# Optimization experiments

Hardware: AMD Instinct MI355X
Metric: run time of the kernel (lower is better)

The kernel has to match this reference:

```python
import jax, jax.numpy as jnp
import numpy as np

NUM_NODES = 50000
NUM_EDGES = 800000
NUM_FEATURES = 128
HIDDEN = 256
NUM_CLASSES = 10
NUM_GRAPHS = 64


def setup_inputs() -> dict:
    key = jax.random.key(0)
    ks = jax.random.split(key, 16)
    x = jax.random.normal(ks[0], (NUM_NODES, NUM_FEATURES), dtype=jnp.float32)
    edge_index = jax.random.randint(ks[1], (2, NUM_EDGES), 0, NUM_NODES, dtype=jnp.int64)
    batch = jnp.sort(jax.random.randint(ks[2], (NUM_NODES,), 0, NUM_GRAPHS, dtype=jnp.int64))

    def glorot(k, shape):
        fan_in, fan_out = shape[-2], shape[-1]
        s = jnp.sqrt(6.0 / (fan_in + fan_out)).astype(jnp.float32)
        return jax.random.uniform(k, shape, jnp.float32, -s, s)

    inp = {
        "x": x, "edge_index": edge_index, "batch": batch,
        # Chebyshev weights: one [in, out] matrix per hop order k
        "W1": glorot(ks[3], (3, NUM_FEATURES, HIDDEN)), "b1": jnp.zeros((HIDDEN,), jnp.float32),
        "W2": glorot(ks[4], (4, HIDDEN, HIDDEN)),       "b2": jnp.zeros((HIDDEN,), jnp.float32),
        "W3": glorot(ks[5], (5, HIDDEN, HIDDEN)),       "b3": jnp.zeros((HIDDEN,), jnp.float32),
        "fc1_w": glorot(ks[6], (HIDDEN, 512)),  "fc1_b": jnp.zeros((512,), jnp.float32),
        "fc2_w": glorot(ks[7], (512, HIDDEN)),  "fc2_b": jnp.zeros((HIDDEN,), jnp.float32),
        "fc3_w": glorot(ks[8], (HIDDEN, NUM_CLASSES)), "fc3_b": jnp.zeros((NUM_CLASSES,), jnp.float32),
    }
    return inp


def reference(x, edge_index, batch, W1, b1, W2, b2, W3, b3,
              fc1_w, fc1_b, fc2_w, fc2_b, fc3_w, fc3_b):
    N = x.shape[0]
    src, dst = edge_index[0], edge_index[1]

    # Scaled Laplacian L_hat = -D^{-1/2} A D^{-1/2} (lambda_max = 2, sym norm)
    deg = jax.ops.segment_sum(jnp.ones_like(src, dtype=x.dtype), src, num_segments=N)
    dis = jnp.where(deg > 0, jax.lax.rsqrt(jnp.maximum(deg, 1.0)), 0.0)
    w = -dis[src] * dis[dst]  # [E]

    def prop(h):  # L_hat @ h via gather-scale-scatter
        return jax.ops.segment_sum(h[src] * w[:, None], dst, num_segments=N)

    def cheb(h, Wk, b):
        K = Wk.shape[0]
        Tx0 = h
        out = Tx0 @ Wk[0]
        Tx1 = prop(h)
        out = out + Tx1 @ Wk[1]
        for k in range(2, K):
            Tx2 = 2.0 * prop(Tx1) - Tx0
            out = out + Tx2 @ Wk[k]
            Tx0, Tx1 = Tx1, Tx2
        return out + b

    h = jax.nn.relu(cheb(x, W1, b1))
    h = jax.nn.relu(cheb(h, W2, b2))
    h = jax.nn.relu(cheb(h, W3, b3))

    # global mean pool over graphs in the batch
    sums = jax.ops.segment_sum(h, batch, num_segments=NUM_GRAPHS)
    cnts = jax.ops.segment_sum(jnp.ones((N,), h.dtype), batch, num_segments=NUM_GRAPHS)
    g = sums / jnp.maximum(cnts, 1.0)[:, None]  # [G, 256]

    g = jax.nn.relu(g @ fc1_w + fc1_b)  # dropout is identity at inference
    g = jax.nn.relu(g @ fc2_w + fc2_b)
    g = g @ fc3_w + fc3_b
    return jax.nn.log_softmax(g, axis=1)
```

## Files before the change

### kernel.cpp

```cpp
#include <hip/hip_runtime.h>
#include <cstdint>
#include <cstddef>

#define NN 50000
#define NE 800000
#define FIN 128
#define HID 256
#define NCLS 10
#define NG 64
#define LDT 1280

#define NCH 13
#define NCELL (NN * NCH)
#define NSCB ((NCELL + 255) / 256)

typedef unsigned int uint;
typedef unsigned short ushort;
typedef __attribute__((ext_vector_type(8))) short short8;
typedef __attribute__((ext_vector_type(4))) float f32x4;

static inline size_t align_up(size_t v, size_t a) { return (v + a - 1) / a * a; }

__device__ __forceinline__ float bf2f(ushort u) {
    union { uint i; float f; } v; v.i = (uint)u << 16; return v.f;
}
__device__ __forceinline__ ushort f2bf(float f) {
    union { uint i; float f; } v; v.f = f;
    uint i = v.i;
    uint r = (i + 0x7fffu + ((i >> 16) & 1u)) >> 16;
    return (ushort)r;
}
__device__ __forceinline__ uint pack2(float a, float b) {
    return (uint)f2bf(a) | ((uint)f2bf(b) << 16);
}


__global__ void k_degcnt(const int* __restrict__ src, const int* __restrict__ dst,
                         int* __restrict__ ideg, int* __restrict__ cellcnt) {
    int e = blockIdx.x * 256 + threadIdx.x;
    if (e < NE) {
        int s = src[e], d = dst[e];
        atomicAdd(&ideg[s], 1);
        atomicAdd(&cellcnt[d * NCH + (s >> 12)], 1);
    }
}

__global__ void k_dis(const int* __restrict__ ideg, float* __restrict__ dis) {
    int n = blockIdx.x * 256 + threadIdx.x;
    if (n < NN) {
        int d = ideg[n];
        dis[n] = (d > 0) ? rsqrtf((float)d) : 0.0f;
    }
}

__global__ void k_scanA(const int* __restrict__ cnt, int* __restrict__ rp,
                        int* __restrict__ bsum) {
    __shared__ int s[256];
    int i = blockIdx.x * 256 + threadIdx.x;
    int v = (i < NCELL) ? cnt[i] : 0;
    s[threadIdx.x] = v;
    __syncthreads();
    for (int off = 1; off < 256; off <<= 1) {
        int t = (threadIdx.x >= (unsigned)off) ? s[threadIdx.x - off] : 0;
        __syncthreads();
        s[threadIdx.x] += t;
        __syncthreads();
    }
    if (i < NCELL) rp[i] = s[threadIdx.x] - v;
    if (threadIdx.x == 255) bsum[blockIdx.x] = s[255];
}

__global__ void k_scanB(int* __restrict__ b, int n) {
    __shared__ int s[1024];
    __shared__ int carry;
    if (threadIdx.x == 0) carry = 0;
    __syncthreads();
    for (int base = 0; base < n; base += 1024) {
        int i = base + threadIdx.x;
        int v = (i < n) ? b[i] : 0;
        s[threadIdx.x] = v;
        __syncthreads();
        for (int off = 1; off < 1024; off <<= 1) {
            int t = (threadIdx.x >= (unsigned)off) ? s[threadIdx.x - off] : 0;
            __syncthreads();
            s[threadIdx.x] += t;
            __syncthreads();
        }
        int c = carry;
        if (i < n) b[i] = c + s[threadIdx.x] - v;
        __syncthreads();
        if (threadIdx.x == 0) carry = c + s[1023];
        __syncthreads();
    }
}

__global__ void k_scanC(const int* __restrict__ bsum, int* __restrict__ rp,
                        int* __restrict__ cur, int* __restrict__ rpn) {
    int i = blockIdx.x * 256 + threadIdx.x;
    if (i < NCELL) {
        int v = rp[i] + bsum[blockIdx.x];
        rp[i] = v;
        cur[i] = v;
        if (i % NCH == 0) rpn[i / NCH] = v;
    }
    if (i == 0) rpn[NN] = NE;
}

__global__ void k_fill2(const int* __restrict__ src, const int* __restrict__ dst,
                        const float* __restrict__ dis, int* __restrict__ cur,
                        uint2* __restrict__ em) {
    int e = blockIdx.x * 256 + threadIdx.x;
    if (e < NE) {
        int s = src[e], d = dst[e];
        int pos = atomicAdd(&cur[d * NCH + (s >> 12)], 1);
        uint2 m;
        m.x = (uint)s;
        m.y = __float_as_uint(-dis[s] * dis[d]);
        em[pos] = m;
    }
}

__global__ void k_wtall(const float* __restrict__ W1, const float* __restrict__ W2,
                        const float* __restrict__ W3, ushort* __restrict__ Wt1,
                        ushort* __restrict__ Wt2, ushort* __restrict__ Wt3) {
    int i = blockIdx.x * 256 + threadIdx.x;
    if (i < 384 * 256) {
        int k = i >> 8, n = i & 255;
        Wt1[(size_t)n * 384 + k] = f2bf(W1[i]);
        return;
    }
    i -= 384 * 256;
    if (i < 1024 * 256) {
        int k = i >> 8, n = i & 255;
        Wt2[(size_t)n * 1024 + k] = f2bf(W2[i]);
        return;
    }
    i -= 1024 * 256;
    if (i < 1280 * 256) {
        int k = i >> 8, n = i & 255;
        Wt3[(size_t)n * 1280 + k] = f2bf(W3[i]);
    }
}


__global__ void k_spread_x(const float* __restrict__ x, ushort* __restrict__ T) {
    int i = blockIdx.x * 256 + threadIdx.x;
    if (i < NN * 64) {
        int m = i >> 6, p = i & 63;
        const float* xp = x + (size_t)m * FIN + p * 2;
        uint* tp = (uint*)(T + (size_t)m * LDT) + p;
        *tp = pack2(xp[0], xp[1]);
    }
}

template <int FUSE, int F>
__global__ __launch_bounds__(512) void k_prop3(
    const int* __restrict__ rpn, const uint2* __restrict__ em,
    const ushort* __restrict__ h, const ushort* __restrict__ sub,
    ushort* __restrict__ out) {
    constexpr int NV = (F == 256) ? 4 : 2;
    int wv = __builtin_amdgcn_readfirstlane(threadIdx.x >> 6);
    int d = blockIdx.x * 8 + wv;
    int lane = threadIdx.x & 63;
    int beg = rpn[d], end = rpn[d + 1];
    float a[NV];
#pragma unroll
    for (int j = 0; j < NV; ++j) a[j] = 0.0f;

    int e = beg;
    int nfull = (end - beg) >> 3;
    if (nfull > 0) {
        uint2 mt[8];
#pragma unroll
        for (int u = 0; u < 8; ++u) mt[u] = em[e + u];
        for (int g = 0; g < nfull; ++g) {
            uint2 mtn[8];
            if (F == 256) {
                uint2 gg[8];
#pragma unroll
                for (int u = 0; u < 8; ++u)
                    gg[u] = *((const uint2*)(h + (size_t)mt[u].x * LDT) + lane);
#pragma unroll
                for (int u = 0; u < 8; ++u) {
                    int pe = e + 8 + u; if (pe > end - 1) pe = end - 1;
                    mtn[u] = em[pe];
                }
#pragma unroll
                for (int u = 0; u < 8; ++u) {
                    float wvv = __uint_as_float(mt[u].y);
                    a[0] += wvv * bf2f((ushort)gg[u].x);
                    a[1] += wvv * bf2f((ushort)(gg[u].x >> 16));
                    a[2] += wvv * bf2f((ushort)gg[u].y);
                    a[3] += wvv * bf2f((ushort)(gg[u].y >> 16));
                }
            } else {
                uint gg[8];
#pragma unroll
                for (int u = 0; u < 8; ++u)
                    gg[u] = *((const uint*)(h + (size_t)mt[u].x * LDT) + lane);
#pragma unroll
                for (int u = 0; u < 8; ++u) {
                    int pe = e + 8 + u; if (pe > end - 1) pe = end - 1;
                    mtn[u] = em[pe];
                }
#pragma unroll
                for (int u = 0; u < 8; ++u) {
                    float wvv = __uint_as_float(mt[u].y);
                    a[0] += wvv * bf2f((ushort)gg[u]);
                    a[1] += wvv * bf2f((ushort)(gg[u] >> 16));
                }
            }
#pragma unroll
            for (int u = 0; u < 8; ++u) mt[u] = mtn[u];
            e += 8;
        }
    }
    for (; e + 4 <= end; e += 4) {
        uint2 mt[4];
#pragma unroll
        for (int u = 0; u < 4; ++u) mt[u] = em[e + u];
        if (F == 256) {
            uint2 gg[4];
#pragma unroll
            for (int u = 0; u < 4; ++u)
                gg[u] = *((const uint2*)(h + (size_t)mt[u].x * LDT) + lane);
#pragma unroll
            for (int u = 0; u < 4; ++u) {
                float wvv = __uint_as_float(mt[u].y);
                a[0] += wvv * bf2f((ushort)gg[u].x);
                a[1] += wvv * bf2f((ushort)(gg[u].x >> 16));
                a[2] += wvv * bf2f((ushort)gg[u].y);
                a[3] += wvv * bf2f((ushort)(gg[u].y >> 16));
            }
        } else {
            uint gg[4];
#pragma unroll
            for (int u = 0; u < 4; ++u)
                gg[u] = *((const uint*)(h + (size_t)mt[u].x * LDT) + lane);
#pragma unroll
            for (int u = 0; u < 4; ++u) {
                float wvv = __uint_as_float(mt[u].y);
                a[0] += wvv * bf2f((ushort)gg[u]);
                a[1] += wvv * bf2f((ushort)(gg[u] >> 16));
            }
        }
    }
    for (; e < end; ++e) {
        uint2 m0 = em[e];
        float w0 = __uint_as_float(m0.y);
        if (F == 256) {
            uint2 g0 = *((const uint2*)(h + (size_t)m0.x * LDT) + lane);
            a[0] += w0 * bf2f((ushort)g0.x); a[1] += w0 * bf2f((ushort)(g0.x >> 16));
            a[2] += w0 * bf2f((ushort)g0.y); a[3] += w0 * bf2f((ushort)(g0.y >> 16));
        } else {
            uint g0 = *((const uint*)(h + (size_t)m0.x * LDT) + lane);
            a[0] += w0 * bf2f((ushort)g0); a[1] += w0 * bf2f((ushort)(g0 >> 16));
        }
    }

    if (F == 256) {
        uint2* op = (uint2*)(out + (size_t)d * LDT) + lane;
        if (FUSE) {
            uint2 sv = *((const uint2*)(sub + (size_t)d * LDT) + lane);
            uint2 r;
            r.x = pack2(2.0f * a[0] - bf2f((ushort)sv.x),
                        2.0f * a[1] - bf2f((ushort)(sv.x >> 16)));
            r.y = pack2(2.0f * a[2] - bf2f((ushort)sv.y),
                        2.0f * a[3] - bf2f((ushort)(sv.y >> 16)));
            *op = r;
        } else {
            uint2 r;
            r.x = pack2(a[0], a[1]);
            r.y = pack2(a[2], a[3]);
            *op = r;
        }
    } else {
        uint* op = (uint*)(out + (size_t)d * LDT) + lane;
        if (FUSE) {
            uint sv = *((const uint*)(sub + (size_t)d * LDT) + lane);
            *op = pack2(2.0f * a[0] - bf2f((ushort)sv),
                        2.0f * a[1] - bf2f((ushort)(sv >> 16)));
        } else {
            *op = pack2(a[0], a[1]);
        }
    }
}

template <int K>
__global__ __launch_bounds__(512, 4) void k_mm7(
    const ushort* __restrict__ A, int lda,
    int m0, int m1, int m2, int m3, int m4,
    const ushort* __restrict__ Wt, const float* __restrict__ bias,
    ushort* __restrict__ H, int ldh, int M) {
    constexpr int NT = K / 32;
    __shared__ ushort As[3][128 * 32];
    __shared__ ushort Bs[3][256 * 32];
    int tid = threadIdx.x;
    int lane = tid & 63, w = tid >> 6;
    int wm = w >> 2, wn = w & 3;
    int rowBase = blockIdx.x * 128;
    int srow = lane >> 2;
    int c16 = lane & 3;

    f32x4 acc[4][4];
#pragma unroll
    for (int i = 0; i < 4; ++i)
#pragma unroll
        for (int j = 0; j < 4; ++j) acc[i][j] = (f32x4){0.f, 0.f, 0.f, 0.f};

    auto stage = [&](int t) {
        int kk = t * 32;
        int slot = kk >> 8;
        int coff = (slot == 0 ? m0 : slot == 1 ? m1 : slot == 2 ? m2
                    : slot == 3 ? m3 : m4) + (kk & 255);
        int b = t % 3;
        {
            int r = w * 16 + srow;
            int cs = c16 ^ ((r >> 1) & 3);
            int grow = rowBase + r;
            if (grow > M - 1) grow = M - 1;
            const ushort* gp = A + (size_t)grow * lda + coff + cs * 8;
            __builtin_amdgcn_global_load_lds(
                (const __attribute__((address_space(1))) void*)gp,
                (__attribute__((address_space(3))) void*)((char*)&As[b][0] + w * 1024),
                16, 0, 0);
        }
#pragma unroll
        for (int q = 0; q < 2; ++q) {
            int seg = w * 2 + q;
            int r = seg * 16 + srow;
            int cs = c16 ^ ((r >> 1) & 3);
            const ushort* gp = Wt + (size_t)r * K + kk + cs * 8;
            __builtin_amdgcn_global_load_lds(
                (const __attribute__((address_space(1))) void*)gp,
                (__attribute__((address_space(3))) void*)((char*)&Bs[b][0] + seg * 1024),
                16, 0, 0);
        }
    };

    stage(0);
    stage(1);

    for (int t = 0; t < NT; ++t) {
        if (t + 1 < NT) {
            asm volatile("s_waitcnt vmcnt(3)" ::: "memory");
        } else {
            asm volatile("s_waitcnt vmcnt(0)" ::: "memory");
        }
        __builtin_amdgcn_s_barrier();
        if (t + 2 < NT) stage(t + 2);

        int b = t % 3;
        short8 af[4], bf[4];
#pragma unroll
        for (int mi = 0; mi < 4; ++mi) {
            int r = wm * 64 + mi * 16 + (lane & 15);
            int j = (lane >> 4) ^ ((r >> 1) & 3);
            af[mi] = *(const short8*)((const char*)&As[b][0] + r * 64 + j * 16);
        }
#pragma unroll
        for (int ni = 0; ni < 4; ++ni) {
            int r = wn * 64 + ni * 16 + (lane & 15);
            int j = (lane >> 4) ^ ((r >> 1) & 3);
            bf[ni] = *(const short8*)((const char*)&Bs[b][0] + r * 64 + j * 16);
        }
#pragma unroll
        for (int mi = 0; mi < 4; ++mi)
#pragma unroll
            for (int ni = 0; ni < 4; ++ni)
                acc[mi][ni] = __builtin_amdgcn_mfma_f32_16x16x32_bf16(
                    af[mi], bf[ni], acc[mi][ni], 0, 0, 0);
    }

    int lg = lane >> 4;
    float bv[4];
#pragma unroll
    for (int ni = 0; ni < 4; ++ni)
        bv[ni] = bias[wn * 64 + ni * 16 + (lane & 15)];
#pragma unroll
    for (int mi = 0; mi < 4; ++mi) {
#pragma unroll
        for (int r = 0; r < 4; ++r) {
            int row = rowBase + wm * 64 + mi * 16 + lg * 4 + r;
            if (row >= M) continue;
#pragma unroll
            for (int ni = 0; ni < 4; ++ni) {
                int colL = wn * 64 + ni * 16 + (lane & 15);
                float v = acc[mi][ni][r] + bv[ni];
                v = fmaxf(v, 0.0f);
                H[(size_t)row * ldh + colL] = f2bf(v);
            }
        }
    }
}


__global__ void k_pool(const ushort* __restrict__ h, const int* __restrict__ batch,
                       float* __restrict__ sums, float* __restrict__ cnts) {
    int f = threadIdx.x;
    int n0 = blockIdx.x * 128;
    if (n0 >= NN) return;
    int nEnd = n0 + 128 < NN ? n0 + 128 : NN;
    int cur = batch[n0];
    float acc = 0.0f, c = 0.0f;
    for (int n = n0; n < nEnd; ++n) {
        int b = batch[n];
        if (b != cur) {
            atomicAdd(&sums[cur * HID + f], acc);
            if (f == 0) atomicAdd(&cnts[cur], c);
            acc = 0.0f; c = 0.0f; cur = b;
        }
        acc += bf2f(h[(size_t)n * HID + f]);
        c += 1.0f;
    }
    atomicAdd(&sums[cur * HID + f], acc);
    if (f == 0) atomicAdd(&cnts[cur], c);
}

__global__ void k_gdiv(const float* __restrict__ sums, const float* __restrict__ cnts,
                       float* __restrict__ g) {
    int i = blockIdx.x * 256 + threadIdx.x;
    int b = i >> 8;
    g[i] = sums[i] / fmaxf(cnts[b], 1.0f);
}


template <int RELU>
__global__ void k_fc(const float* __restrict__ in, const float* __restrict__ W,
                     const float* __restrict__ bias, float* __restrict__ out,
                     int K, int Nc) {
    __shared__ float s[512];
    int gi = blockIdx.x;
    for (int i = threadIdx.x; i < K; i += blockDim.x) s[i] = in[gi * K + i];
    __syncthreads();
    int c = blockIdx.y * blockDim.x + threadIdx.x;
    if (c < Nc) {
        float acc = bias[c];
        for (int k = 0; k < K; ++k) acc += s[k] * W[k * Nc + c];
        out[gi * Nc + c] = RELU ? fmaxf(acc, 0.0f) : acc;
    }
}

__global__ void k_fc3_lsm(const float* __restrict__ in, const float* __restrict__ W,
                          const float* __restrict__ b, float* __restrict__ out) {
    __shared__ float s[HID];
    __shared__ float lg[NCLS];
    int gi = blockIdx.x;
    s[threadIdx.x] = in[gi * HID + threadIdx.x];
    __syncthreads();
    if (threadIdx.x < NCLS) {
        float acc = b[threadIdx.x];
        for (int k = 0; k < HID; ++k) acc += s[k] * W[k * NCLS + threadIdx.x];
        lg[threadIdx.x] = acc;
    }
    __syncthreads();
    if (threadIdx.x < NCLS) {
        float m = -1e30f;
        for (int c = 0; c < NCLS; ++c) m = fmaxf(m, lg[c]);
        float sum = 0.0f;
        for (int c = 0; c < NCLS; ++c) sum += expf(lg[c] - m);
        out[gi * NCLS + threadIdx.x] = lg[threadIdx.x] - m - logf(sum);
    }
}


extern "C" void kernel_launch(void* const* d_in, const int* in_sizes, int n_in,
                              void* d_out, int out_size, void* d_ws, size_t ws_size,
                              hipStream_t stream) {
    const float* x = (const float*)d_in[0];
    const int* ei = (const int*)d_in[1];
    const int* src = ei;
    const int* dst = ei + NE;
    const int* batch = (const int*)d_in[2];
    const float* W1 = (const float*)d_in[3];
    const float* b1 = (const float*)d_in[4];
    const float* W2 = (const float*)d_in[5];
    const float* b2 = (const float*)d_in[6];
    const float* W3 = (const float*)d_in[7];
    const float* b3 = (const float*)d_in[8];
    const float* fc1w = (const float*)d_in[9];
    const float* fc1b = (const float*)d_in[10];
    const float* fc2w = (const float*)d_in[11];
    const float* fc2b = (const float*)d_in[12];
    const float* fc3w = (const float*)d_in[13];
    const float* fc3b = (const float*)d_in[14];
    float* out = (float*)d_out;

    char* p = (char*)d_ws;
    auto carve = [&](size_t bytes) {
        char* r = p;
        p += align_up(bytes, 256);
        return (void*)r;
    };
    ushort* Tbig = (ushort*)carve((size_t)NN * LDT * 2);
    ushort* hA = (ushort*)carve((size_t)NN * HID * 2);
    ushort* Wt1 = (ushort*)carve((size_t)HID * 384 * 2);
    ushort* Wt2 = (ushort*)carve((size_t)HID * 1024 * 2);
    ushort* Wt3 = (ushort*)carve((size_t)HID * 1280 * 2);
    int* ideg = (int*)carve((size_t)NN * 4);
    float* dis = (float*)carve((size_t)NN * 4);
    uint2* em = (uint2*)carve((size_t)NE * 8);
    int* cellcnt = (int*)carve((size_t)NCELL * 4);
    int* cellptr = (int*)carve((size_t)(NCELL + 1) * 4);
    int* ccur = (int*)carve((size_t)NCELL * 4);
    int* rpn = (int*)carve((size_t)(NN + 1) * 4);
    int* bsum = (int*)carve((size_t)NSCB * 4);
    float* psum = (float*)carve((size_t)NG * HID * 4);
    float* pcnt = (float*)carve((size_t)NG * 4);
    float* g = (float*)carve((size_t)NG * HID * 4);
    float* f1 = (float*)carve((size_t)NG * 512 * 4);
    float* f2 = (float*)carve((size_t)NG * HID * 4);

    hipMemsetAsync(ideg, 0, (size_t)NN * 4, stream);
    hipMemsetAsync(cellcnt, 0, (size_t)NCELL * 4, stream);
    hipMemsetAsync(psum, 0, (size_t)NG * HID * 4, stream);
    hipMemsetAsync(pcnt, 0, (size_t)NG * 4, stream);

    k_degcnt<<<(NE + 255) / 256, 256, 0, stream>>>(src, dst, ideg, cellcnt);
    k_dis<<<(NN + 255) / 256, 256, 0, stream>>>(ideg, dis);
    k_scanA<<<NSCB, 256, 0, stream>>>(cellcnt, cellptr, bsum);
    k_scanB<<<1, 1024, 0, stream>>>(bsum, NSCB);
    k_scanC<<<NSCB, 256, 0, stream>>>(bsum, cellptr, ccur, rpn);
    k_fill2<<<(NE + 255) / 256, 256, 0, stream>>>(src, dst, dis, ccur, em);

    k_wtall<<<(384 + 1024 + 1280), 256, 0, stream>>>(W1, W2, W3, Wt1, Wt2, Wt3);

    int mmg = (NN + 127) / 128;

    k_spread_x<<<(NN * 64 + 255) / 256, 256, 0, stream>>>(x, Tbig);
    k_prop3<0, 128><<<NN / 8, 512, 0, stream>>>(rpn, em, Tbig + 0, nullptr, Tbig + 128);
    k_prop3<1, 128><<<NN / 8, 512, 0, stream>>>(rpn, em, Tbig + 128, Tbig + 0, Tbig + 256);
    k_mm7<384><<<mmg, 512, 0, stream>>>(Tbig, LDT, 0, 256, 0, 0, 0,
                                        Wt1, b1, Tbig + 1024, LDT, NN);

    k_prop3<0, 256><<<NN / 8, 512, 0, stream>>>(rpn, em, Tbig + 1024, nullptr, Tbig + 0);
    k_prop3<1, 256><<<NN / 8, 512, 0, stream>>>(rpn, em, Tbig + 0, Tbig + 1024, Tbig + 256);
    k_prop3<1, 256><<<NN / 8, 512, 0, stream>>>(rpn, em, Tbig + 256, Tbig + 0, Tbig + 512);
    k_mm7<1024><<<mmg, 512, 0, stream>>>(Tbig, LDT, 1024, 0, 256, 512, 0,
                                         Wt2, b2, Tbig + 768, LDT, NN);

    k_prop3<0, 256><<<NN / 8, 512, 0, stream>>>(rpn, em, Tbig + 768, nullptr, Tbig + 1024);
    k_prop3<1, 256><<<NN / 8, 512, 0, stream>>>(rpn, em, Tbig + 1024, Tbig + 768, Tbig + 0);
    k_prop3<1, 256><<<NN / 8, 512, 0, stream>>>(rpn, em, Tbig + 0, Tbig + 1024, Tbig + 256);
    k_prop3<1, 256><<<NN / 8, 512, 0, stream>>>(rpn, em, Tbig + 256, Tbig + 0, Tbig + 512);
    k_mm7<1280><<<mmg, 512, 0, stream>>>(Tbig, LDT, 768, 1024, 0, 256, 512,
                                         Wt3, b3, hA, HID, NN);

    k_pool<<<(NN + 127) / 128, 256, 0, stream>>>(hA, batch, psum, pcnt);
    k_gdiv<<<(NG * HID) / 256, 256, 0, stream>>>(psum, pcnt, g);
    k_fc<1><<<dim3(NG, 2), 256, 0, stream>>>(g, fc1w, fc1b, f1, HID, 512);
    k_fc<1><<<dim3(NG, 1), 256, 0, stream>>>(f1, fc2w, fc2b, f2, 512, HID);
    k_fc3_lsm<<<NG, 256, 0, stream>>>(f2, fc3w, fc3b, out);
}
```

Measured before the change: 799.7 us.

## Shrink edge metadata to source indices and split 256-wide propagation across two waves

Edges now store only the source index. The per-edge weight is rebuilt in the propagation kernels from dis[src] and a per-destination -dis[d] factor applied once after accumulation. Cell counters and cursors are packed as 16-bit halves of 32-bit words, halving their footprint and removing the cursor copy in the scan. The 256-feature propagation gives each destination two wavefronts, each handling 128 features with 32-bit gathers and a deeper 16-edge unroll, which doubles the grid. The changes trade per-edge metadata bandwidth for an extra dependent gather of dis per edge, and the 16-bit counters assume no cell exceeds 65535 edges.

After: 1.136 ms. +42.1%, slower.

```diff
diff --git a/kernel.cpp b/kernel.cpp
--- a/kernel.cpp
+++ b/kernel.cpp
@@ -36,12 +36,13 @@
 
 
 __global__ void k_degcnt(const int* __restrict__ src, const int* __restrict__ dst,
-                         int* __restrict__ ideg, int* __restrict__ cellcnt) {
+                         int* __restrict__ ideg, uint* __restrict__ cellcnt32) {
     int e = blockIdx.x * 256 + threadIdx.x;
     if (e < NE) {
         int s = src[e], d = dst[e];
         atomicAdd(&ideg[s], 1);
-        atomicAdd(&cellcnt[d * NCH + (s >> 12)], 1);
+        int cell = d * NCH + (s >> 12);
+        atomicAdd(&cellcnt32[cell >> 1], 1u << ((cell & 1) * 16));
     }
 }
 
@@ -53,11 +54,12 @@
     }
 }
 
-__global__ void k_scanA(const int* __restrict__ cnt, int* __restrict__ rp,
+__global__ void k_scanA(const uint* __restrict__ cnt32, int* __restrict__ rp,
                         int* __restrict__ bsum) {
     __shared__ int s[256];
     int i = blockIdx.x * 256 + threadIdx.x;
-    int v = (i < NCELL) ? cnt[i] : 0;
+    int v = 0;
+    if (i < NCELL) v = (int)((cnt32[i >> 1] >> ((i & 1) * 16)) & 0xffffu);
     s[threadIdx.x] = v;
     __syncthreads();
     for (int off = 1; off < 256; off <<= 1) {
@@ -95,28 +97,26 @@
 }
 
 __global__ void k_scanC(const int* __restrict__ bsum, int* __restrict__ rp,
-                        int* __restrict__ cur, int* __restrict__ rpn) {
+                        int* __restrict__ rpn) {
     int i = blockIdx.x * 256 + threadIdx.x;
     if (i < NCELL) {
         int v = rp[i] + bsum[blockIdx.x];
         rp[i] = v;
-        cur[i] = v;
         if (i % NCH == 0) rpn[i / NCH] = v;
     }
     if (i == 0) rpn[NN] = NE;
 }
 
 __global__ void k_fill2(const int* __restrict__ src, const int* __restrict__ dst,
-                        const float* __restrict__ dis, int* __restrict__ cur,
-                        uint2* __restrict__ em) {
+                        const int* __restrict__ cellptr, uint* __restrict__ cur32,
+                        uint* __restrict__ em) {
     int e = blockIdx.x * 256 + threadIdx.x;
     if (e < NE) {
         int s = src[e], d = dst[e];
-        int pos = atomicAdd(&cur[d * NCH + (s >> 12)], 1);
-        uint2 m;
-        m.x = (uint)s;
-        m.y = __float_as_uint(-dis[s] * dis[d]);
-        em[pos] = m;
+        int cell = d * NCH + (s >> 12);
+        uint old = atomicAdd(&cur32[cell >> 1], 1u << ((cell & 1) * 16));
+        int loc = (int)((old >> ((cell & 1) * 16)) & 0xffffu);
+        em[cellptr[cell] + loc] = (uint)s;
     }
 }
 
@@ -153,136 +153,117 @@
     }
 }
 
-template <int FUSE, int F>
-__global__ __launch_bounds__(512) void k_prop3(
-    const int* __restrict__ rpn, const uint2* __restrict__ em,
-    const ushort* __restrict__ h, const ushort* __restrict__ sub,
-    ushort* __restrict__ out) {
-    constexpr int NV = (F == 256) ? 4 : 2;
-    int wv = __builtin_amdgcn_readfirstlane(threadIdx.x >> 6);
-    int d = blockIdx.x * 8 + wv;
+template <int FUSE>
+__global__ __launch_bounds__(512) void k_prop256(
+    const int* __restrict__ rpn, const uint* __restrict__ em,
+    const float* __restrict__ dis, const ushort* __restrict__ h,
+    const ushort* __restrict__ sub, ushort* __restrict__ out) {
+    int tid = threadIdx.x;
+    int d = blockIdx.x * 4 + (tid >> 7);
+    int half = (tid >> 6) & 1;
+    int lane = tid & 63;
+    int cidx = half * 64 + lane;
+    int beg = rpn[d], end = rpn[d + 1];
+    float disd = -dis[d];
+    float a0 = 0.0f, a1 = 0.0f;
+
+    int e = beg;
+    int nfull = (end - beg) >> 4;
+    for (int g = 0; g < nfull; ++g) {
+        int sv[16]; float ds[16]; uint gg[16];
+#pragma unroll
+        for (int u = 0; u < 16; ++u) sv[u] = (int)em[e + u];
+#pragma unroll
+        for (int u = 0; u < 16; ++u) ds[u] = dis[sv[u]];
+#pragma unroll
+        for (int u = 0; u < 16; ++u)
+            gg[u] = *((const uint*)(h + (size_t)sv[u] * LDT) + cidx);
+#pragma unroll
+        for (int u = 0; u < 16; ++u) {
+            a0 += ds[u] * bf2f((ushort)gg[u]);
+            a1 += ds[u] * bf2f((ushort)(gg[u] >> 16));
+        }
+        e += 16;
+    }
+    for (; e + 4 <= end; e += 4) {
+        int sv[4]; float ds[4]; uint gg[4];
+#pragma unroll
+        for (int u = 0; u < 4; ++u) sv[u] = (int)em[e + u];
+#pragma unroll
+        for (int u = 0; u < 4; ++u) ds[u] = dis[sv[u]];
+#pragma unroll
+        for (int u = 0; u < 4; ++u)
+            gg[u] = *((const uint*)(h + (size_t)sv[u] * LDT) + cidx);
+#pragma unroll
+        for (int u = 0; u < 4; ++u) {
+            a0 += ds[u] * bf2f((ushort)gg[u]);
+            a1 += ds[u] * bf2f((ushort)(gg[u] >> 16));
+        }
+    }
+    for (; e < end; ++e) {
+        int s = (int)em[e];
+        float dsv = dis[s];
+        uint g0 = *((const uint*)(h + (size_t)s * LDT) + cidx);
+        a0 += dsv * bf2f((ushort)g0);
+        a1 += dsv * bf2f((ushort)(g0 >> 16));
+    }
+
+    a0 *= disd; a1 *= disd;
+    uint* op = (uint*)(out + (size_t)d * LDT) + cidx;
+    if (FUSE) {
+        uint sv = *((const uint*)(sub + (size_t)d * LDT) + cidx);
+        *op = pack2(2.0f * a0 - bf2f((ushort)sv),
+                    2.0f * a1 - bf2f((ushort)(sv >> 16)));
+    } else {
+        *op = pack2(a0, a1);
+    }
+}
+
+template <int FUSE>
+__global__ __launch_bounds__(512) void k_prop128(
+    const int* __restrict__ rpn, const uint* __restrict__ em,
+    const float* __restrict__ dis, const ushort* __restrict__ h,
+    const ushort* __restrict__ sub, ushort* __restrict__ out) {
+    int d = blockIdx.x * 8 + (threadIdx.x >> 6);
     int lane = threadIdx.x & 63;
     int beg = rpn[d], end = rpn[d + 1];
-    float a[NV];
-#pragma unroll
-    for (int j = 0; j < NV; ++j) a[j] = 0.0f;
+    float disd = -dis[d];
+    float a0 = 0.0f, a1 = 0.0f;
 
     int e = beg;
     int nfull = (end - beg) >> 3;
-    if (nfull > 0) {
-        uint2 mt[8];
-#pragma unroll
-        for (int u = 0; u < 8; ++u) mt[u] = em[e + u];
-        for (int g = 0; g < nfull; ++g) {
-            uint2 mtn[8];
-            if (F == 256) {
-                uint2 gg[8];
-#pragma unroll
-                for (int u = 0; u < 8; ++u)
-                    gg[u] = *((const uint2*)(h + (size_t)mt[u].x * LDT) + lane);
-#pragma unroll
-                for (int u = 0; u < 8; ++u) {
-                    int pe = e + 8 + u; if (pe > end - 1) pe = end - 1;
-                    mtn[u] = em[pe];
-                }
-#pragma unroll
-                for (int u = 0; u < 8; ++u) {
-                    float wvv = __uint_as_float(mt[u].y);
-                    a[0] += wvv * bf2f((ushort)gg[u].x);
-                    a[1] += wvv * bf2f((ushort)(gg[u].x >> 16));
-                    a[2] += wvv * bf2f((ushort)gg[u].y);
-                    a[3] += wvv * bf2f((ushort)(gg[u].y >> 16));
-                }
-            } else {
-                uint gg[8];
-#pragma unroll
-                for (int u = 0; u < 8; ++u)
-                    gg[u] = *((const uint*)(h + (size_t)mt[u].x * LDT) + lane);
-#pragma unroll
-                for (int u = 0; u < 8; ++u) {
-                    int pe = e + 8 + u; if (pe > end - 1) pe = end - 1;
-                    mtn[u] = em[pe];
-                }
-#pragma unroll
-                for (int u = 0; u < 8; ++u) {
-                    float wvv = __uint_as_float(mt[u].y);
-                    a[0] += wvv * bf2f((ushort)gg[u]);
-                    a[1] += wvv * bf2f((ushort)(gg[u] >> 16));
-                }
-            }
-#pragma unroll
-            for (int u = 0; u < 8; ++u) mt[u] = mtn[u];
-            e += 8;
-        }
-    }
-    for (; e + 4 <= end; e += 4) {
-        uint2 mt[4];
-#pragma unroll
-        for (int u = 0; u < 4; ++u) mt[u] = em[e + u];
-        if (F == 256) {
-            uint2 gg[4];
-#pragma unroll
-            for (int u = 0; u < 4; ++u)
-                gg[u] = *((const uint2*)(h + (size_t)mt[u].x * LDT) + lane);
-#pragma unroll
-            for (int u = 0; u < 4; ++u) {
-                float wvv = __uint_as_float(mt[u].y);
-                a[0] += wvv * bf2f((ushort)gg[u].x);
-                a[1] += wvv * bf2f((ushort)(gg[u].x >> 16));
-                a[2] += wvv * bf2f((ushort)gg[u].y);
-                a[3] += wvv * bf2f((ushort)(gg[u].y >> 16));
-            }
-        } else {
-            uint gg[4];
-#pragma unroll
-            for (int u = 0; u < 4; ++u)
-                gg[u] = *((const uint*)(h + (size_t)mt[u].x * LDT) + lane);
-#pragma unroll
-            for (int u = 0; u < 4; ++u) {
-                float wvv = __uint_as_float(mt[u].y);
-                a[0] += wvv * bf2f((ushort)gg[u]);
-                a[1] += wvv * bf2f((ushort)(gg[u] >> 16));
-            }
-        }
+    for (int g = 0; g < nfull; ++g) {
+        int sv[8]; float ds[8]; uint gg[8];
+#pragma unroll
+        for (int u = 0; u < 8; ++u) sv[u] = (int)em[e + u];
+#pragma unroll
+        for (int u = 0; u < 8; ++u) ds[u] = dis[sv[u]];
+#pragma unroll
+        for (int u = 0; u < 8; ++u)
+            gg[u] = *((const uint*)(h + (size_t)sv[u] * LDT) + lane);
+#pragma unroll
+        for (int u = 0; u < 8; ++u) {
+            a0 += ds[u] * bf2f((ushort)gg[u]);
+            a1 += ds[u] * bf2f((ushort)(gg[u] >> 16));
+        }
+        e += 8;
     }
     for (; e < end; ++e) {
-        uint2 m0 = em[e];
-        float w0 = __uint_as_float(m0.y);
-        if (F == 256) {
-            uint2 g0 = *((const uint2*)(h + (size_t)m0.x * LDT) + lane);
-            a[0] += w0 * bf2f((ushort)g0.x); a[1] += w0 * bf2f((ushort)(g0.x >> 16));
-            a[2] += w0 * bf2f((ushort)g0.y); a[3] += w0 * bf2f((ushort)(g0.y >> 16));
-        } else {
-            uint g0 = *((const uint*)(h + (size_t)m0.x * LDT) + lane);
-            a[0] += w0 * bf2f((ushort)g0); a[1] += w0 * bf2f((ushort)(g0 >> 16));
-        }
-    }
-
-    if (F == 256) {
-        uint2* op = (uint2*)(out + (size_t)d * LDT) + lane;
-        if (FUSE) {
-            uint2 sv = *((const uint2*)(sub + (size_t)d * LDT) + lane);
-            uint2 r;
-            r.x = pack2(2.0f * a[0] - bf2f((ushort)sv.x),
-                        2.0f * a[1] - bf2f((ushort)(sv.x >> 16)));
-            r.y = pack2(2.0f * a[2] - bf2f((ushort)sv.y),
-                        2.0f * a[3] - bf2f((ushort)(sv.y >> 16)));
-            *op = r;
-        } else {
-            uint2 r;
-            r.x = pack2(a[0], a[1]);
-            r.y = pack2(a[2], a[3]);
-            *op = r;
-        }
+        int s = (int)em[e];
+        float dsv = dis[s];
+        uint g0 = *((const uint*)(h + (size_t)s * LDT) + lane);
+        a0 += dsv * bf2f((ushort)g0);
+        a1 += dsv * bf2f((ushort)(g0 >> 16));
+    }
+
+    a0 *= disd; a1 *= disd;
+    uint* op = (uint*)(out + (size_t)d * LDT) + lane;
+    if (FUSE) {
+        uint sv = *((const uint*)(sub + (size_t)d * LDT) + lane);
+        *op = pack2(2.0f * a0 - bf2f((ushort)sv),
+                    2.0f * a1 - bf2f((ushort)(sv >> 16)));
     } else {
-        uint* op = (uint*)(out + (size_t)d * LDT) + lane;
-        if (FUSE) {
-            uint sv = *((const uint*)(sub + (size_t)d * LDT) + lane);
-            *op = pack2(2.0f * a[0] - bf2f((ushort)sv),
-                        2.0f * a[1] - bf2f((ushort)(sv >> 16)));
-        } else {
-            *op = pack2(a[0], a[1]);
-        }
+        *op = pack2(a0, a1);
     }
 }
 
@@ -499,10 +480,10 @@
     ushort* Wt3 = (ushort*)carve((size_t)HID * 1280 * 2);
     int* ideg = (int*)carve((size_t)NN * 4);
     float* dis = (float*)carve((size_t)NN * 4);
-    uint2* em = (uint2*)carve((size_t)NE * 8);
-    int* cellcnt = (int*)carve((size_t)NCELL * 4);
+    uint* em = (uint*)carve((size_t)NE * 4);
+    uint* cellcnt32 = (uint*)carve((size_t)NCELL * 2);
     int* cellptr = (int*)carve((size_t)(NCELL + 1) * 4);
-    int* ccur = (int*)carve((size_t)NCELL * 4);
+    uint* cur32 = (uint*)carve((size_t)NCELL * 2);
     int* rpn = (int*)carve((size_t)(NN + 1) * 4);
     int* bsum = (int*)carve((size_t)NSCB * 4);
     float* psum = (float*)carve((size_t)NG * HID * 4);
@@ -512,37 +493,38 @@
     float* f2 = (float*)carve((size_t)NG * HID * 4);
 
     hipMemsetAsync(ideg, 0, (size_t)NN * 4, stream);
-    hipMemsetAsync(cellcnt, 0, (size_t)NCELL * 4, stream);
+    hipMemsetAsync(cellcnt32, 0, (size_t)NCELL * 2, stream);
+    hipMemsetAsync(cur32, 0, (size_t)NCELL * 2, stream);
     hipMemsetAsync(psum, 0, (size_t)NG * HID * 4, stream);
     hipMemsetAsync(pcnt, 0, (size_t)NG * 4, stream);
 
-    k_degcnt<<<(NE + 255) / 256, 256, 0, stream>>>(src, dst, ideg, cellcnt);
+    k_degcnt<<<(NE + 255) / 256, 256, 0, stream>>>(src, dst, ideg, cellcnt32);
     k_dis<<<(NN + 255) / 256, 256, 0, stream>>>(ideg, dis);
-    k_scanA<<<NSCB, 256, 0, stream>>>(cellcnt, cellptr, bsum);
+    k_scanA<<<NSCB, 256, 0, stream>>>(cellcnt32, cellptr, bsum);
     k_scanB<<<1, 1024, 0, stream>>>(bsum, NSCB);
-    k_scanC<<<NSCB, 256, 0, stream>>>(bsum, cellptr, ccur, rpn);
-    k_fill2<<<(NE + 255) / 256, 256, 0, stream>>>(src, dst, dis, ccur, em);
+    k_scanC<<<NSCB, 256, 0, stream>>>(bsum, cellptr, rpn);
+    k_fill2<<<(NE + 255) / 256, 256, 0, stream>>>(src, dst, cellptr, cur32, em);
 
     k_wtall<<<(384 + 1024 + 1280), 256, 0, stream>>>(W1, W2, W3, Wt1, Wt2, Wt3);
 
     int mmg = (NN + 127) / 128;
 
     k_spread_x<<<(NN * 64 + 255) / 256, 256, 0, stream>>>(x, Tbig);
-    k_prop3<0, 128><<<NN / 8, 512, 0, stream>>>(rpn, em, Tbig + 0, nullptr, Tbig + 128);
-    k_prop3<1, 128><<<NN / 8, 512, 0, stream>>>(rpn, em, Tbig + 128, Tbig + 0, Tbig + 256);
+    k_prop128<0><<<NN / 8, 512, 0, stream>>>(rpn, em, dis, Tbig + 0, nullptr, Tbig + 128);
+    k_prop128<1><<<NN / 8, 512, 0, stream>>>(rpn, em, dis, Tbig + 128, Tbig + 0, Tbig + 256);
     k_mm7<384><<<mmg, 512, 0, stream>>>(Tbig, LDT, 0, 256, 0, 0, 0,
                                         Wt1, b1, Tbig + 1024, LDT, NN);
 
-    k_prop3<0, 256><<<NN / 8, 512, 0, stream>>>(rpn, em, Tbig + 1024, nullptr, Tbig + 0);
-    k_prop3<1, 256><<<NN / 8, 512, 0, stream>>>(rpn, em, Tbig + 0, Tbig + 1024, Tbig + 256);
-    k_prop3<1, 256><<<NN / 8, 512, 0, stream>>>(rpn, em, Tbig + 256, Tbig + 0, Tbig + 512);
+    k_prop256<0><<<NN / 4, 512, 0, stream>>>(rpn, em, dis, Tbig + 1024, nullptr, Tbig + 0);
+    k_prop256<1><<<NN / 4, 512, 0, stream>>>(rpn, em, dis, Tbig + 0, Tbig + 1024, Tbig + 256);
+    k_prop256<1><<<NN / 4, 512, 0, stream>>>(rpn, em, dis, Tbig + 256, Tbig + 0, Tbig + 512);
     k_mm7<1024><<<mmg, 512, 0, stream>>>(Tbig, LDT, 1024, 0, 256, 512, 0,
                                          Wt2, b2, Tbig + 768, LDT, NN);
 
-    k_prop3<0, 256><<<NN / 8, 512, 0, stream>>>(rpn, em, Tbig + 768, nullptr, Tbig + 1024);
-    k_prop3<1, 256><<<NN / 8, 512, 0, stream>>>(rpn, em, Tbig + 1024, Tbig + 768, Tbig + 0);
-    k_prop3<1, 256><<<NN / 8, 512, 0, stream>>>(rpn, em, Tbig + 0, Tbig + 1024, Tbig + 256);
-    k_prop3<1, 256><<<NN / 8, 512, 0, stream>>>(rpn, em, Tbig + 256, Tbig + 0, Tbig + 512);
+    k_prop256<0><<<NN / 4, 512, 0, stream>>>(rpn, em, dis, Tbig + 768, nullptr, Tbig + 1024);
+    k_prop256<1><<<NN / 4, 512, 0, stream>>>(rpn, em, dis, Tbig + 1024, Tbig + 768, Tbig + 0);
+    k_prop256<1><<<NN / 4, 512, 0, stream>>>(rpn, em, dis, Tbig + 0, Tbig + 1024, Tbig + 256);
+    k_prop256<1><<<NN / 4, 512, 0, stream>>>(rpn, em, dis, Tbig + 256, Tbig + 0, Tbig + 512);
     k_mm7<1280><<<mmg, 512, 0, stream>>>(Tbig, LDT, 768, 1024, 0, 256, 512,
                                          Wt3, b3, hA, HID, NN);
 
```
